# Kernel tuning notes

Measured on AMD Instinct MI355X. Metric: run time of the kernel, lower is better.

## Reference

```python
import jax, jax.numpy as jnp
import numpy as np

# Dims: B=2, S=2048, D=1024 hidden, E=8 experts, F=2752 ffn (SwiGLU), top-1 gate,
# capacity_factor=1.0 -> capacity C = (B*S)//E = 512. Residual-MoE (moe_use_residual=True).

def setup_inputs() -> dict:
    key = jax.random.key(0)
    ks = jax.random.split(key, 10)
    B, S, D, E, F = 2, 2048, 1024, 8, 2752
    sc = 0.02
    return {
        "hidden_states": jax.random.normal(ks[0], (B, S, D), jnp.float32),
        "wg":  jax.random.normal(ks[1], (D, E), jnp.float32) * sc,   # gate
        "w1":  jax.random.normal(ks[2], (E, D, F), jnp.float32) * sc,  # expert SwiGLU
        "w3":  jax.random.normal(ks[3], (E, D, F), jnp.float32) * sc,
        "w2":  jax.random.normal(ks[4], (E, F, D), jnp.float32) * sc,
        "rw1": jax.random.normal(ks[5], (D, F), jnp.float32) * sc,    # residual MLP (SwiGLU, no bias)
        "rw3": jax.random.normal(ks[6], (D, F), jnp.float32) * sc,
        "rw2": jax.random.normal(ks[7], (F, D), jnp.float32) * sc,
        "cw":  jax.random.normal(ks[8], (D, 2), jnp.float32) * sc,    # coefficient Linear(D, 2)
        "cb":  jnp.zeros((2,), jnp.float32),
    }


def _moe_forward(x, wg, w1, w3, w2):
    """GShard/DeepSpeed-style top-1 gated MoE with capacity + token dropping.
    x: [T, D] flattened tokens. Returns (out [T,D], l_aux scalar, exp_counts [E])."""
    T, D = x.shape
    E = wg.shape[1]
    C = max(4, T // E)  # capacity_factor = 1.0, min_capacity = 4

    logits = x @ wg                                  # [T, E]
    gates = jax.nn.softmax(logits, axis=-1)
    idx = jnp.argmax(gates, axis=-1)                 # top-1 expert per token
    mask1 = jax.nn.one_hot(idx, E, dtype=gates.dtype)  # [T, E]
    exp_counts = jnp.sum(mask1, axis=0).astype(jnp.int32)

    # load-balancing aux loss (DeepSpeed top1gating)
    me = jnp.mean(gates, axis=0)
    ce = jnp.mean(mask1, axis=0)
    l_aux = jnp.sum(me * ce) * E

    # position of each token within its expert's buffer; drop overflow
    locations = jnp.cumsum(mask1, axis=0) - 1.0      # [T, E]
    mask1 = mask1 * (locations < C)
    loc_s = jnp.sum(locations * mask1, axis=1).astype(jnp.int32)  # [T]
    gates1 = jnp.sum(gates * mask1, axis=1)          # [T] gate weight (0 if dropped)

    loc_oh = jax.nn.one_hot(loc_s, C, dtype=gates.dtype)          # [T, C]
    combine = gates1[:, None, None] * mask1[:, :, None] * loc_oh[:, None, :]  # [T, E, C]
    dispatch = (combine > 0).astype(x.dtype)

    xe = jnp.einsum("tec,td->ecd", dispatch, x)      # dispatch to [E, C, D]
    h = jax.nn.silu(jnp.einsum("ecd,edf->ecf", xe, w1)) * jnp.einsum("ecd,edf->ecf", xe, w3)
    ye = jnp.einsum("ecf,efd->ecd", h, w2)           # expert SwiGLU FFN
    out = jnp.einsum("tec,ecd->td", combine, ye)     # weighted combine back to tokens
    return out, l_aux, exp_counts


def reference(hidden_states, wg, w1, w3, w2, rw1, rw3, rw2, cw, cb):
    B, S, D = hidden_states.shape
    x = hidden_states.reshape(-1, D)
    moe_out, l_aux, exp_counts = _moe_forward(x, wg, w1, w3, w2)
    moe_out = moe_out.reshape(B, S, D)

    # residual SwiGLU MLP + softmax-gated combine (Residual-MoE)
    mlp = (jax.nn.silu(hidden_states @ rw1) * (hidden_states @ rw3)) @ rw2
    coef = jax.nn.softmax(hidden_states @ cw + cb, axis=-1)  # [B, S, 2]
    output = moe_out * coef[..., 0:1] + mlp * coef[..., 1:2]
    return output, l_aux, exp_counts
```

## Files before the change

kernel.cpp:

```cpp
#include <hip/hip_runtime.h>
#include <hip/hip_bf16.h>
#include <stdint.h>

#define T_TOK 4096
#define DD 1024
#define EE 8
#define CC 512
#define FF 2752

typedef __attribute__((ext_vector_type(8))) short bf16x8;
typedef __attribute__((ext_vector_type(4))) float f32x4;
typedef __attribute__((ext_vector_type(4))) unsigned short us4;
typedef __attribute__((ext_vector_type(8))) unsigned short us8;

__device__ __forceinline__ float bf2f(unsigned short u) {
  union { float f; unsigned int i; } v; v.i = ((unsigned int)u) << 16; return v.f;
}
__device__ __forceinline__ unsigned short f2bf(float f) {
  union { float f; unsigned int i; } v; v.f = f;
  unsigned int r = v.i + 0x7fffu + ((v.i >> 16) & 1u);
  return (unsigned short)(r >> 16);
}

#define GLDS16(g, l) __builtin_amdgcn_global_load_lds( \
    (const __attribute__((address_space(1))) void*)(g), \
    (__attribute__((address_space(3))) void*)(l), 16, 0, 0)

#define STG_CHUNK(l) (((l & 3) ^ ((l >> 3) & 3)) * 8)
#define RD_OFF(fr, fq) ((fr) * 32 + (((fq) ^ (((fr) >> 1) & 3)) * 8))

#define BAR() do { asm volatile("" ::: "memory"); __builtin_amdgcn_s_barrier(); \
                   asm volatile("" ::: "memory"); } while (0)

template<int RT>
__global__ __launch_bounds__(256)
void transpose_k(const float* __restrict__ in, const float* __restrict__ in2,
                 unsigned short* __restrict__ out, unsigned short* __restrict__ out2,
                 int R, int C, long inStride, long outStride) {
  __shared__ unsigned short sm[RT * 64];
  int b = blockIdx.z;
  if (b < EE) { in += (long)b * inStride; out += (long)b * outStride; }
  else { in = in2; out = out2; }
  int cb = blockIdx.x * 64, rb = blockIdx.y * RT;
  int t = threadIdx.x;
  int rr = t >> 4, c4 = (t & 15) * 4;
#pragma unroll
  for (int i = 0; i < RT / 16; ++i) {
    int r = rr + i * 16;
    float4 v = *(const float4*)(in + (long)(rb + r) * C + cb + c4);
    us4 o; o.x = f2bf(v.x); o.y = f2bf(v.y); o.z = f2bf(v.z); o.w = f2bf(v.w);
    *(us4*)&sm[r * 64 + (c4 ^ (((r >> 3) & 7) << 3))] = o;
  }
  __syncthreads();
#pragma unroll
  for (int j = 0; j < (64 * (RT / 8)) / 256; ++j) {
    int idx = t + j * 256;
    int g, c;
    if (RT == 128) { g = idx & 15; c = idx >> 4; }
    else           { g = idx & 7;  c = idx >> 3; }
    int r8 = g * 8;
    us8 o;
#pragma unroll
    for (int k = 0; k < 8; ++k) {
      int r = r8 + k;
      o[k] = sm[r * 64 + (c ^ (((r >> 3) & 7) << 3))];
    }
    *(us8*)(out + (long)(cb + c) * R + rb + r8) = o;
  }
}

__global__ void zero_me_k(float* me) { if (threadIdx.x < EE) me[threadIdx.x] = 0.0f; }

__global__ void gate_k(const float* __restrict__ x, const float* __restrict__ wg,
                       const float* __restrict__ cw, const float* __restrict__ cbv,
                       int* __restrict__ idx, float* __restrict__ gatev,
                       float* __restrict__ coef, float* __restrict__ me_sum) {
  int tid = threadIdx.x, lane = tid & 63, wv = tid >> 6;
  int t = blockIdx.x * 4 + wv;
  const float* xr = x + (long)t * DD;
  float acc[EE] = {0,0,0,0,0,0,0,0};
  float c0 = 0.0f, c1 = 0.0f;
  for (int d = lane; d < DD; d += 64) {
    float xv = xr[d];
#pragma unroll
    for (int e = 0; e < EE; ++e) acc[e] += xv * wg[d * EE + e];
    c0 += xv * cw[d * 2 + 0];
    c1 += xv * cw[d * 2 + 1];
  }
#pragma unroll
  for (int o = 32; o > 0; o >>= 1) {
#pragma unroll
    for (int e = 0; e < EE; ++e) acc[e] += __shfl_xor(acc[e], o);
    c0 += __shfl_xor(c0, o);
    c1 += __shfl_xor(c1, o);
  }
  __shared__ float sme[EE];
  if (tid < EE) sme[tid] = 0.0f;
  __syncthreads();
  if (lane == 0) {
    float m = acc[0]; int am = 0;
#pragma unroll
    for (int e = 1; e < EE; ++e) if (acc[e] > m) { m = acc[e]; am = e; }
    float g[EE]; float s = 0.0f;
#pragma unroll
    for (int e = 0; e < EE; ++e) { g[e] = __expf(acc[e] - m); s += g[e]; }
    float inv = 1.0f / s;
    idx[t] = am;
    gatev[t] = g[am] * inv;
#pragma unroll
    for (int e = 0; e < EE; ++e) atomicAdd(&sme[e], g[e] * inv);
    float l0 = c0 + cbv[0], l1 = c1 + cbv[1];
    float mm = fmaxf(l0, l1);
    float e0 = __expf(l0 - mm), e1 = __expf(l1 - mm);
    float is = 1.0f / (e0 + e1);
    coef[t * 2 + 0] = e0 * is;
    coef[t * 2 + 1] = e1 * is;
  }
  __syncthreads();
  if (tid < EE) atomicAdd(&me_sum[tid], sme[tid]);
}

__global__ void scan_k(const int* __restrict__ idx, const float* __restrict__ me_sum,
                       int* __restrict__ slot, int* __restrict__ tok,
                       float* __restrict__ out_tail) {
  __shared__ int sidx[T_TOK];
  __shared__ int counts[EE];
  int tid = threadIdx.x;
  for (int i = tid; i < T_TOK; i += 512) sidx[i] = idx[i];
  __syncthreads();
  int e = tid >> 6, lane = tid & 63;
  int base = 0;
  for (int it = 0; it < T_TOK / 64; ++it) {
    int t = it * 64 + lane;
    bool f = (sidx[t] == e);
    unsigned long long m = __ballot(f);
    if (f) {
      int loc = base + __popcll(m & ((1ull << lane) - 1ull));
      slot[t] = (loc < CC) ? loc : -1;
      if (loc < CC) tok[e * CC + loc] = t;
    }
    base += __popcll(m);
  }
  if (lane == 0) counts[e] = base;
  __syncthreads();
  int filled = min(counts[e], CC);
  for (int c = filled + lane; c < CC; c += 64) tok[e * CC + c] = -1;
  if (tid == 0) {
    float la = 0.0f;
    for (int i = 0; i < EE; ++i) la += me_sum[i] * (float)counts[i];
    la *= (float)EE / ((float)T_TOK * (float)T_TOK);
    out_tail[0] = la;
    for (int i = 0; i < EE; ++i) out_tail[1 + i] = (float)counts[i];
  }
}

__global__ void gather_k(const float* __restrict__ x, const int* __restrict__ tok,
                         unsigned short* __restrict__ xb, unsigned short* __restrict__ xe) {
  int r = blockIdx.x, tid = threadIdx.x;
  int d = tid * 4;
  if (r < T_TOK) {
    float4 v = *(const float4*)(x + (long)r * DD + d);
    us4 o; o.x = f2bf(v.x); o.y = f2bf(v.y); o.z = f2bf(v.z); o.w = f2bf(v.w);
    *(us4*)(xb + (long)r * DD + d) = o;
  } else {
    int s = r - T_TOK;
    int t = tok[s];
    us4 o = {0, 0, 0, 0};
    if (t >= 0) {
      float4 v = *(const float4*)(x + (long)t * DD + d);
      o.x = f2bf(v.x); o.y = f2bf(v.y); o.z = f2bf(v.z); o.w = f2bf(v.w);
    }
    *(us4*)(xe + (long)s * DD + d) = o;
  }
}

__global__ __launch_bounds__(512, 2)
void gemm1_k(const unsigned short* __restrict__ xcat,
             const float* __restrict__ w1, const float* __restrict__ w3,
             const float* __restrict__ rw1, const float* __restrict__ rw3,
             unsigned short* __restrict__ Hcat) {
  int lin = blockIdx.x;
  int work = (lin & 7) * 88 + (lin >> 3);
  int mtile, ntile;
  if (work < 352) {
    int e = work / 44, r = work - e * 44;
    ntile = r >> 1;
    mtile = e * 2 + (r & 1);
  } else {
    int q = work - 352;
    ntile = q >> 4;
    mtile = 16 + (q & 15);
  }
  const unsigned short* A = xcat + (size_t)mtile * 256 * DD;
  const float *B1, *B3;
  if (mtile < 16) { int e = mtile >> 1; B1 = w1 + (size_t)e * DD * FF; B3 = w3 + (size_t)e * DD * FF; }
  else { B1 = rw1; B3 = rw3; }
  unsigned short* H = Hcat + (size_t)mtile * 256 * FF;
  int n0 = ntile * 128;

  __shared__ __align__(16) char Lc[147456];
  const unsigned short* ldsS = (const unsigned short*)Lc;

  int tid = threadIdx.x, l = tid & 63, w = tid >> 6;
  int wm = w >> 1, wn = w & 1;
  int fr = l & 15, fq = l >> 4;
  int srow = l >> 2, soff = STG_CHUNK(l);
  int rdo = RD_OFF(fr, fq);

  const unsigned short* gA0 = A + (size_t)(w * 16 + srow) * DD + soff;
  const unsigned short* gA1 = A + (size_t)((8 + w) * 16 + srow) * DD + soff;
  int lrow = l >> 5;
  int kl0 = 2 * w + lrow;
  int kl1 = 16 + 2 * w + lrow;
  int cs0 = (l & 31) ^ (((kl0 >> 3) & 1) << 2);
  int cs1 = (l & 31) ^ (((kl1 >> 3) & 1) << 2);
  int nn0 = n0 + 4 * cs0; if (nn0 >= FF) nn0 = 0;
  int nn1 = n0 + 4 * cs1; if (nn1 >= FF) nn1 = 0;
  const float* gB1a = B1 + (size_t)kl0 * FF + nn0;
  const float* gB1b = B1 + (size_t)kl1 * FF + nn1;
  const float* gB3a = B3 + (size_t)kl0 * FF + nn0;
  const float* gB3b = B3 + (size_t)kl1 * FF + nn1;

  int cb[4];
#pragma unroll
  for (int ni = 0; ni < 4; ++ni)
    cb[ni] = fq * 4096 + ((((wn * 4 + ni) * 64 + fr * 4)) ^ ((fq & 1) << 6));

#define STG1(bb, hw) do { size_t ka = (size_t)(hw) * 32; size_t kb = ka * FF;   \
    GLDS16(gA0 + ka, Lc + (bb) * 16384 + w * 1024);                             \
    GLDS16(gA1 + ka, Lc + (bb) * 16384 + (8 + w) * 1024);                       \
    GLDS16(gB1a + kb, Lc + 49152 + (bb) * 16384 + w * 1024);                    \
    GLDS16(gB1b + kb, Lc + 49152 + (bb) * 16384 + (8 + w) * 1024);              \
    GLDS16(gB3a + kb, Lc + 98304 + (bb) * 16384 + w * 1024);                    \
    GLDS16(gB3b + kb, Lc + 98304 + (bb) * 16384 + (8 + w) * 1024); } while (0)

  f32x4 acc1[4][4] = {};
  f32x4 acc3[4][4] = {};

  const int HN = 32;
  STG1(0, 0);
  STG1(1, 1);

  for (int h = 0; h < HN; ++h) {
    int buf = h % 3;
    int hw = h + 2; if (hw >= HN) hw -= HN;
    int bufw = (buf + 2) % 3;

    asm volatile("s_waitcnt vmcnt(6)" ::: "memory");
    BAR();
    STG1(bufw, hw);

    const char* Bb1 = Lc + 49152 + buf * 16384;
    const char* Bb3 = Lc + 98304 + buf * 16384;
    bf16x8 af[4];
#pragma unroll
    for (int mi = 0; mi < 4; ++mi)
      af[mi] = *(const bf16x8*)(ldsS + buf * 8192 + (wm * 4 + mi) * 512 + rdo);

    {
      float fb[4][8];
#pragma unroll
      for (int ni = 0; ni < 4; ++ni)
#pragma unroll
        for (int j = 0; j < 8; ++j)
          fb[ni][j] = *(const float*)(Bb1 + cb[ni] + j * 512);
      __builtin_amdgcn_s_setprio(1);
#pragma unroll
      for (int ni = 0; ni < 4; ++ni) {
        union { bf16x8 h; unsigned int u[4]; } bu;
#pragma unroll
        for (int p = 0; p < 4; ++p)
          asm("v_cvt_pk_bf16_f32 %0, %1, %2" : "=v"(bu.u[p]) : "v"(fb[ni][2 * p]), "v"(fb[ni][2 * p + 1]));
#pragma unroll
        for (int mi = 0; mi < 4; ++mi)
          acc1[mi][ni] = __builtin_amdgcn_mfma_f32_16x16x32_bf16(af[mi], bu.h, acc1[mi][ni], 0, 0, 0);
      }
      __builtin_amdgcn_s_setprio(0);
    }
    {
      float fb[4][8];
#pragma unroll
      for (int ni = 0; ni < 4; ++ni)
#pragma unroll
        for (int j = 0; j < 8; ++j)
          fb[ni][j] = *(const float*)(Bb3 + cb[ni] + j * 512);
      __builtin_amdgcn_s_setprio(1);
#pragma unroll
      for (int ni = 0; ni < 4; ++ni) {
        union { bf16x8 h; unsigned int u[4]; } bu;
#pragma unroll
        for (int p = 0; p < 4; ++p)
          asm("v_cvt_pk_bf16_f32 %0, %1, %2" : "=v"(bu.u[p]) : "v"(fb[ni][2 * p]), "v"(fb[ni][2 * p + 1]));
#pragma unroll
        for (int mi = 0; mi < 4; ++mi)
          acc3[mi][ni] = __builtin_amdgcn_mfma_f32_16x16x32_bf16(af[mi], bu.h, acc3[mi][ni], 0, 0, 0);
      }
      __builtin_amdgcn_s_setprio(0);
    }
  }
#undef STG1

#pragma unroll
  for (int mi = 0; mi < 4; ++mi)
#pragma unroll
    for (int ni = 0; ni < 4; ++ni)
#pragma unroll
      for (int r = 0; r < 4; ++r) {
        int gm = wm * 64 + mi * 16 + fq * 4 + r;
        int gn = n0 + wn * 64 + ni * 16 + fr;
        if (gn < FF) {
          float v1 = acc1[mi][ni][r], v3 = acc3[mi][ni][r];
          float h = v1 / (1.0f + __expf(-v1)) * v3;
          H[(size_t)gm * FF + gn] = f2bf(h);
        }
      }
}

__global__ __launch_bounds__(512, 2)
void gemm2_k(const unsigned short* __restrict__ Hcat,
             const unsigned short* __restrict__ w2t, const unsigned short* __restrict__ rw2t,
             unsigned short* __restrict__ Ycat) {
  int lin = blockIdx.x;
  int work = (lin & 7) * 32 + (lin >> 3);
  int mtile, ntile;
  if (work < 128) {
    int e = work >> 4, r = work & 15;
    ntile = r >> 1;
    mtile = e * 2 + (r & 1);
  } else {
    int q = work - 128;
    ntile = q >> 4;
    mtile = 16 + (q & 15);
  }
  const unsigned short* A = Hcat + (size_t)mtile * 256 * FF;
  const unsigned short* B = (mtile < 16) ? (w2t + (size_t)(mtile >> 1) * (size_t)DD * FF) : rw2t;
  unsigned short* Y = Ycat + (size_t)mtile * 256 * DD;
  int n0 = ntile * 128;

  __shared__ __align__(16) unsigned short lds[73728];
  char* Lc = (char*)lds;

  int tid = threadIdx.x, l = tid & 63, w = tid >> 6;
  int wm = w >> 1, wn = w & 1;
  int fr = l & 15, fq = l >> 4;
  int srow = l >> 2, soff = STG_CHUNK(l);
  int rdo = RD_OFF(fr, fq);

  const unsigned short* gA0 = A + (size_t)(w * 16 + srow) * FF + soff;
  const unsigned short* gA1 = A + (size_t)((8 + w) * 16 + srow) * FF + soff;
  const unsigned short* gB  = B + (size_t)(n0 + w * 16 + srow) * FF + soff;

#define STG2(bb, kk) do {                                          \
    GLDS16(gA0 + (kk), Lc + (bb) * 16384 + w * 1024);              \
    GLDS16(gA1 + (kk), Lc + (bb) * 16384 + (8 + w) * 1024);        \
    GLDS16(gB  + (kk), Lc + 98304 + (bb) * 8192 + w * 1024); } while (0)

  f32x4 acc[4][4] = {};

  const int HN = 86;
#pragma unroll
  for (int hh = 0; hh < 5; ++hh) STG2(hh, hh * 32);
  asm volatile("s_waitcnt vmcnt(12)" ::: "memory");
  BAR();

  int b = 0;
#pragma unroll 2
  for (int h = 0; h < HN; ++h) {
    int bn = b ? b - 1 : 5;
    int hw = h + 5; if (hw >= HN) hw -= HN;
    int kk = hw * 32;
    bf16x8 af[4], bf[4];

#pragma unroll
    for (int mi = 0; mi < 4; ++mi)
      af[mi] = *(const bf16x8*)(lds + b * 8192 + (wm * 4 + mi) * 512 + rdo);
#pragma unroll
    for (int ni = 0; ni < 4; ++ni)
      bf[ni] = *(const bf16x8*)(lds + 49152 + b * 4096 + (wn * 4 + ni) * 512 + rdo);
    STG2(bn, kk);
    asm volatile("s_waitcnt vmcnt(12)" ::: "memory");
    BAR();
    __builtin_amdgcn_s_setprio(1);
#pragma unroll
    for (int mi = 0; mi < 4; ++mi)
#pragma unroll
      for (int ni = 0; ni < 4; ++ni)
        acc[mi][ni] = __builtin_amdgcn_mfma_f32_16x16x32_bf16(af[mi], bf[ni], acc[mi][ni], 0, 0, 0);
    __builtin_amdgcn_s_setprio(0);
    BAR();

    ++b; if (b == 6) b = 0;
  }
#undef STG2

#pragma unroll
  for (int mi = 0; mi < 4; ++mi)
#pragma unroll
    for (int ni = 0; ni < 4; ++ni)
#pragma unroll
      for (int r = 0; r < 4; ++r) {
        int gm = wm * 64 + mi * 16 + fq * 4 + r;
        int gn = n0 + wn * 64 + ni * 16 + fr;
        Y[(size_t)gm * DD + gn] = f2bf(acc[mi][ni][r]);
      }
}

__global__ void combine_k(const unsigned short* __restrict__ Ye, const unsigned short* __restrict__ Yr,
                          const int* __restrict__ idx, const int* __restrict__ slot,
                          const float* __restrict__ gatev, const float* __restrict__ coef,
                          float* __restrict__ out) {
  int t = blockIdx.x, tid = threadIdx.x;
  int d = tid * 4;
  float c0 = coef[t * 2], c1 = coef[t * 2 + 1];
  int s = slot[t];
  float g = gatev[t] * c0;
  us4 vr = *(const us4*)(Yr + (size_t)t * DD + d);
  float4 o;
  if (s >= 0) {
    us4 ve = *(const us4*)(Ye + ((size_t)idx[t] * CC + s) * DD + d);
    o.x = g * bf2f(ve.x) + c1 * bf2f(vr.x);
    o.y = g * bf2f(ve.y) + c1 * bf2f(vr.y);
    o.z = g * bf2f(ve.z) + c1 * bf2f(vr.z);
    o.w = g * bf2f(ve.w) + c1 * bf2f(vr.w);
  } else {
    o.x = c1 * bf2f(vr.x);
    o.y = c1 * bf2f(vr.y);
    o.z = c1 * bf2f(vr.z);
    o.w = c1 * bf2f(vr.w);
  }
  *(float4*)(out + (size_t)t * DD + d) = o;
}

extern "C" void kernel_launch(void* const* d_in, const int* in_sizes, int n_in,
                              void* d_out, int out_size, void* d_ws, size_t ws_size,
                              hipStream_t stream) {
  const float* x   = (const float*)d_in[0];
  const float* wg  = (const float*)d_in[1];
  const float* w1  = (const float*)d_in[2];
  const float* w3  = (const float*)d_in[3];
  const float* w2  = (const float*)d_in[4];
  const float* rw1 = (const float*)d_in[5];
  const float* rw3 = (const float*)d_in[6];
  const float* rw2 = (const float*)d_in[7];
  const float* cw  = (const float*)d_in[8];
  const float* cbv = (const float*)d_in[9];
  float* out = (float*)d_out;

  char* ws = (char*)d_ws;
  size_t o = 0;
  auto alloc = [&](size_t bytes) -> char* {
    char* p = ws + o; o = (o + bytes + 255) & ~(size_t)255; return p;
  };
  unsigned short* w2t  = (unsigned short*)alloc((size_t)EE * DD * FF * 2);
  unsigned short* rw2t = (unsigned short*)alloc((size_t)DD * FF * 2);
  unsigned short* xe   = (unsigned short*)alloc((size_t)T_TOK * DD * 2);
  unsigned short* xb   = (unsigned short*)alloc((size_t)T_TOK * DD * 2);
  unsigned short* He   = (unsigned short*)alloc((size_t)T_TOK * FF * 2);
  unsigned short* Hr   = (unsigned short*)alloc((size_t)T_TOK * FF * 2);
  unsigned short* Ye   = (unsigned short*)alloc((size_t)T_TOK * DD * 2);
  unsigned short* Yr   = (unsigned short*)alloc((size_t)T_TOK * DD * 2);
  int*   idxp  = (int*)alloc(T_TOK * 4);
  float* gatev = (float*)alloc(T_TOK * 4);
  int*   slotp = (int*)alloc(T_TOK * 4);
  int*   tokp  = (int*)alloc(EE * CC * 4);
  float* coefp = (float*)alloc(T_TOK * 2 * 4);
  float* mep   = (float*)alloc(256);
  if (o > ws_size) return;

  transpose_k<64><<<dim3(16, 43, EE + 1), 256, 0, stream>>>(w2, rw2, w2t, rw2t, FF, DD, (long)FF * DD, (long)DD * FF);

  zero_me_k<<<1, 64, 0, stream>>>(mep);
  gate_k<<<T_TOK / 4, 256, 0, stream>>>(x, wg, cw, cbv, idxp, gatev, coefp, mep);
  scan_k<<<1, 512, 0, stream>>>(idxp, mep, slotp, tokp, out + (size_t)T_TOK * DD);
  gather_k<<<2 * T_TOK, 256, 0, stream>>>(x, tokp, xb, xe);
  gemm1_k<<<704, 512, 0, stream>>>(xe, w1, w3, rw1, rw3, He);
  gemm2_k<<<256, 512, 0, stream>>>(He, w2t, rw2t, Ye);
  combine_k<<<T_TOK, 256, 0, stream>>>(Ye, Yr, idxp, slotp, gatev, coefp, out);
}
```

Before: 271.4 us.

## Stage fp32 expert weights through registers, store bf16 to LDS

The up-projection GEMM used to copy fp32 w1/w3 tiles straight into LDS with direct global-to-LDS loads and convert them to bf16 on every MFMA read. It now loads those tiles into registers, converts them to bf16 once, and writes them to a swizzled LDS layout. This halves B-tile LDS use (from 144KB to 96KB) and lets the inner loop read packed bf16x8 fragments directly. The cost is extra VGPRs for the in-flight float4 loads and a more delicate vmcnt/lgkmcnt pipeline that ties register staging to the triple buffer.

```diff
diff --git a/kernel.cpp b/kernel.cpp
--- a/kernel.cpp
+++ b/kernel.cpp
@@ -198,107 +198,133 @@
   unsigned short* H = Hcat + (size_t)mtile * 256 * FF;
   int n0 = ntile * 128;
 
-  __shared__ __align__(16) char Lc[147456];
-  const unsigned short* ldsS = (const unsigned short*)Lc;
+  __shared__ __align__(16) char Lc[98304];
 
   int tid = threadIdx.x, l = tid & 63, w = tid >> 6;
   int wm = w >> 1, wn = w & 1;
   int fr = l & 15, fq = l >> 4;
   int srow = l >> 2, soff = STG_CHUNK(l);
-  int rdo = RD_OFF(fr, fq);
+  int rdo2 = RD_OFF(fr, fq) * 2;
+
+  int chB = fr * 64 + ((fq ^ ((fr >> 1) & 3) ^ ((fr >> 2) & 3)) * 16);
 
   const unsigned short* gA0 = A + (size_t)(w * 16 + srow) * DD + soff;
   const unsigned short* gA1 = A + (size_t)((8 + w) * 16 + srow) * DD + soff;
-  int lrow = l >> 5;
-  int kl0 = 2 * w + lrow;
-  int kl1 = 16 + 2 * w + lrow;
-  int cs0 = (l & 31) ^ (((kl0 >> 3) & 1) << 2);
-  int cs1 = (l & 31) ^ (((kl1 >> 3) & 1) << 2);
-  int nn0 = n0 + 4 * cs0; if (nn0 >= FF) nn0 = 0;
-  int nn1 = n0 + 4 * cs1; if (nn1 >= FF) nn1 = 0;
-  const float* gB1a = B1 + (size_t)kl0 * FF + nn0;
-  const float* gB1b = B1 + (size_t)kl1 * FF + nn1;
-  const float* gB3a = B3 + (size_t)kl0 * FF + nn0;
-  const float* gB3b = B3 + (size_t)kl1 * FF + nn1;
-
-  int cb[4];
-#pragma unroll
-  for (int ni = 0; ni < 4; ++ni)
-    cb[ni] = fq * 4096 + ((((wn * 4 + ni) * 64 + fr * 4)) ^ ((fq & 1) << 6));
-
-#define STG1(bb, hw) do { size_t ka = (size_t)(hw) * 32; size_t kb = ka * FF;   \
-    GLDS16(gA0 + ka, Lc + (bb) * 16384 + w * 1024);                             \
-    GLDS16(gA1 + ka, Lc + (bb) * 16384 + (8 + w) * 1024);                       \
-    GLDS16(gB1a + kb, Lc + 49152 + (bb) * 16384 + w * 1024);                    \
-    GLDS16(gB1b + kb, Lc + 49152 + (bb) * 16384 + (8 + w) * 1024);              \
-    GLDS16(gB3a + kb, Lc + 98304 + (bb) * 16384 + w * 1024);                    \
-    GLDS16(gB3b + kb, Lc + 98304 + (bb) * 16384 + (8 + w) * 1024); } while (0)
+
+  int kp = l >> 5, c = l & 31;
+  int nn = n0 + c * 4; if (nn >= FF) nn = 0;
+  const float* pB1 = B1 + (size_t)(w * 4 + kp * 2) * FF + nn;
+  const float* pB3 = B3 + (size_t)(w * 4 + kp * 2) * FF + nn;
+
+  int fq_w = w >> 1, j_w = (w & 1) * 4 + kp * 2;
+  int frg = c >> 2;
+  int wboff[4];
+#pragma unroll
+  for (int i = 0; i < 4; ++i) {
+    int frw = 4 * (c & 3) + i;
+    int chw = fq_w ^ ((frw >> 1) & 3) ^ ((frw >> 2) & 3);
+    wboff[i] = (frg * 1024 + frw * 64 + chw * 16 + j_w * 2) ^ ((frg & 1) << 6);
+  }
+
+  auto agld = [&](int bb, int hw) {
+    size_t ka = (size_t)hw * 32;
+    GLDS16(gA0 + ka, Lc + bb * 16384 + w * 1024);
+    GLDS16(gA1 + ka, Lc + bb * 16384 + (8 + w) * 1024);
+  };
+  auto bload = [&](int hw, float4& ra, float4& rb, float4& rc, float4& rd) {
+    size_t kb = (size_t)hw * 32 * FF;
+    ra = *(const float4*)(pB1 + kb);
+    rb = *(const float4*)(pB1 + kb + FF);
+    rc = *(const float4*)(pB3 + kb);
+    rd = *(const float4*)(pB3 + kb + FF);
+  };
+  auto bwrite = [&](int bb, float4& ra, float4& rb, float4& rc, float4& rd) {
+    char* b1d = Lc + 49152 + bb * 8192;
+    char* b3d = Lc + 73728 + bb * 8192;
+    const float* fa = (const float*)&ra; const float* fb = (const float*)&rb;
+    const float* fc = (const float*)&rc; const float* fd = (const float*)&rd;
+#pragma unroll
+    for (int i = 0; i < 4; ++i) {
+      unsigned int u;
+      asm("v_cvt_pk_bf16_f32 %0, %1, %2" : "=v"(u) : "v"(fa[i]), "v"(fb[i]));
+      *(unsigned int*)(b1d + wboff[i]) = u;
+    }
+#pragma unroll
+    for (int i = 0; i < 4; ++i) {
+      unsigned int u;
+      asm("v_cvt_pk_bf16_f32 %0, %1, %2" : "=v"(u) : "v"(fc[i]), "v"(fd[i]));
+      *(unsigned int*)(b3d + wboff[i]) = u;
+    }
+  };
 
   f32x4 acc1[4][4] = {};
   f32x4 acc3[4][4] = {};
-
+  bf16x8 af[4], bfB[4];
+
+  auto readA = [&](int bb) {
+#pragma unroll
+    for (int mi = 0; mi < 4; ++mi)
+      af[mi] = *(const bf16x8*)(Lc + bb * 16384 + (wm * 4 + mi) * 1024 + rdo2);
+  };
+  auto readB = [&](int rbase, int bb) {
+#pragma unroll
+    for (int ni = 0; ni < 4; ++ni) {
+      int g = wn * 4 + ni;
+      bfB[ni] = *(const bf16x8*)(Lc + rbase + bb * 8192 + ((g * 1024 + chB) ^ ((g & 1) << 6)));
+    }
+  };
+  auto mm1 = [&]() {
+    __builtin_amdgcn_s_setprio(1);
+#pragma unroll
+    for (int mi = 0; mi < 4; ++mi)
+#pragma unroll
+      for (int ni = 0; ni < 4; ++ni)
+        acc1[mi][ni] = __builtin_amdgcn_mfma_f32_16x16x32_bf16(af[mi], bfB[ni], acc1[mi][ni], 0, 0, 0);
+    __builtin_amdgcn_s_setprio(0);
+  };
+  auto mm3 = [&]() {
+    __builtin_amdgcn_s_setprio(1);
+#pragma unroll
+    for (int mi = 0; mi < 4; ++mi)
+#pragma unroll
+      for (int ni = 0; ni < 4; ++ni)
+        acc3[mi][ni] = __builtin_amdgcn_mfma_f32_16x16x32_bf16(af[mi], bfB[ni], acc3[mi][ni], 0, 0, 0);
+    __builtin_amdgcn_s_setprio(0);
+  };
+
+  float4 s0a, s0b, s0c, s0d, s1a, s1b, s1c, s1d;
   const int HN = 32;
-  STG1(0, 0);
-  STG1(1, 1);
-
+
+  bload(0, s0a, s0b, s0c, s0d);
+  agld(0, 0);
+  bload(1, s1a, s1b, s1c, s1d);
+  agld(1, 1);
+  asm volatile("s_waitcnt vmcnt(8)" ::: "memory");
+  bwrite(0, s0a, s0b, s0c, s0d);
+  asm volatile("s_waitcnt vmcnt(6)" ::: "memory");
+  asm volatile("s_waitcnt lgkmcnt(0)" ::: "memory");
+
+#pragma unroll 2
   for (int h = 0; h < HN; ++h) {
     int buf = h % 3;
-    int hw = h + 2; if (hw >= HN) hw -= HN;
-    int bufw = (buf + 2) % 3;
-
+    int buf1 = (h + 1) % 3;
+    int hw2 = h + 2; if (hw2 >= HN) hw2 -= HN;
+    int buf2 = hw2 % 3;
+
+    BAR();
+    readA(buf);
+    readB(49152, buf);
+    if ((h & 1) == 0) bload(hw2, s0a, s0b, s0c, s0d);
+    else              bload(hw2, s1a, s1b, s1c, s1d);
+    agld(buf2, hw2);
+    mm1();
+    readB(73728, buf);
+    mm3();
     asm volatile("s_waitcnt vmcnt(6)" ::: "memory");
-    BAR();
-    STG1(bufw, hw);
-
-    const char* Bb1 = Lc + 49152 + buf * 16384;
-    const char* Bb3 = Lc + 98304 + buf * 16384;
-    bf16x8 af[4];
-#pragma unroll
-    for (int mi = 0; mi < 4; ++mi)
-      af[mi] = *(const bf16x8*)(ldsS + buf * 8192 + (wm * 4 + mi) * 512 + rdo);
-
-    {
-      float fb[4][8];
-#pragma unroll
-      for (int ni = 0; ni < 4; ++ni)
-#pragma unroll
-        for (int j = 0; j < 8; ++j)
-          fb[ni][j] = *(const float*)(Bb1 + cb[ni] + j * 512);
-      __builtin_amdgcn_s_setprio(1);
-#pragma unroll
-      for (int ni = 0; ni < 4; ++ni) {
-        union { bf16x8 h; unsigned int u[4]; } bu;
-#pragma unroll
-        for (int p = 0; p < 4; ++p)
-          asm("v_cvt_pk_bf16_f32 %0, %1, %2" : "=v"(bu.u[p]) : "v"(fb[ni][2 * p]), "v"(fb[ni][2 * p + 1]));
-#pragma unroll
-        for (int mi = 0; mi < 4; ++mi)
-          acc1[mi][ni] = __builtin_amdgcn_mfma_f32_16x16x32_bf16(af[mi], bu.h, acc1[mi][ni], 0, 0, 0);
-      }
-      __builtin_amdgcn_s_setprio(0);
-    }
-    {
-      float fb[4][8];
-#pragma unroll
-      for (int ni = 0; ni < 4; ++ni)
-#pragma unroll
-        for (int j = 0; j < 8; ++j)
-          fb[ni][j] = *(const float*)(Bb3 + cb[ni] + j * 512);
-      __builtin_amdgcn_s_setprio(1);
-#pragma unroll
-      for (int ni = 0; ni < 4; ++ni) {
-        union { bf16x8 h; unsigned int u[4]; } bu;
-#pragma unroll
-        for (int p = 0; p < 4; ++p)
-          asm("v_cvt_pk_bf16_f32 %0, %1, %2" : "=v"(bu.u[p]) : "v"(fb[ni][2 * p]), "v"(fb[ni][2 * p + 1]));
-#pragma unroll
-        for (int mi = 0; mi < 4; ++mi)
-          acc3[mi][ni] = __builtin_amdgcn_mfma_f32_16x16x32_bf16(af[mi], bu.h, acc3[mi][ni], 0, 0, 0);
-      }
-      __builtin_amdgcn_s_setprio(0);
-    }
-  }
-#undef STG1
+    if ((h & 1) == 0) bwrite(buf1, s1a, s1b, s1c, s1d);
+    else              bwrite(buf1, s0a, s0b, s0c, s0d);
+    asm volatile("s_waitcnt lgkmcnt(0)" ::: "memory");
+  }
 
 #pragma unroll
   for (int mi = 0; mi < 4; ++mi)
```

Measured after the change: 290.8 us. 1.07x slower.
